# Optimization experiments

Hardware: AMD Instinct MI355X
Metric: run time of the kernel (lower is better)

Reference implementation:

```python
import jax, jax.numpy as jnp
import numpy as np
from jax import lax

N, H, W, C = 4, 64, 64, 256
G, K = 8, 3
Cg = C // G
PAD, STRIDE, DIL = 1, 1, 1
OFFSET_SCALE = 1.0
P = K * K


def setup_inputs() -> dict:
    key = jax.random.key(0)
    ks = jax.random.split(key, 12)
    s = 1.0 / np.sqrt(C)
    return {
        "x": jax.random.normal(ks[0], (N, H, W, C), jnp.float32),
        "in_w": jax.random.normal(ks[1], (C, C), jnp.float32) * s,
        "in_b": jnp.zeros((C,), jnp.float32),
        "out_w": jax.random.normal(ks[2], (C, C), jnp.float32) * s,
        "out_b": jnp.zeros((C,), jnp.float32),
        "off_w": jax.random.normal(ks[3], (C, G * P * 2), jnp.float32) * 0.02,
        "off_b": jax.random.normal(ks[4], (G * P * 2,), jnp.float32) * 0.1,
        "mask_w": jax.random.normal(ks[5], (C, G * P), jnp.float32) * 0.02,
        "mask_b": jnp.zeros((G * P,), jnp.float32),
        "dw_k": jax.random.normal(ks[6], (C, 1, K, K), jnp.float32) * (1.0 / K),
        "bn_g": 1.0 + 0.1 * jax.random.normal(ks[7], (C,), jnp.float32),
        "bn_b": 0.1 * jax.random.normal(ks[8], (C,), jnp.float32),
        "bn_m": 0.1 * jax.random.normal(ks[9], (C,), jnp.float32),
        "bn_v": 1.0 + 0.1 * jax.random.uniform(ks[10], (C,), jnp.float32),
    }


def _bilinear_sample(img, grid):
    # img: [B, Cc, Hi, Wi]; grid: [B, L, P, 2], (x, y) in [-1, 1]
    # grid_sample(mode='bilinear', padding_mode='zeros', align_corners=False)
    B, Cc, Hi, Wi = img.shape
    x = ((grid[..., 0] + 1.0) * Wi - 1.0) * 0.5
    y = ((grid[..., 1] + 1.0) * Hi - 1.0) * 0.5
    x0 = jnp.floor(x)
    y0 = jnp.floor(y)
    fx = x - x0
    fy = y - y0
    x0i = x0.astype(jnp.int32)
    y0i = y0.astype(jnp.int32)
    flat = img.reshape(B, Cc, Hi * Wi)
    gather = jax.vmap(lambda f, i: f[:, i])  # [Cc,HW], [L,P] -> [Cc,L,P]

    def corner(xc, yc, w):
        valid = (xc >= 0) & (xc < Wi) & (yc >= 0) & (yc < Hi)
        idx = jnp.clip(yc, 0, Hi - 1) * Wi + jnp.clip(xc, 0, Wi - 1)
        return gather(flat, idx) * (w * valid)[:, None]

    out = corner(x0i, y0i, (1.0 - fx) * (1.0 - fy))
    out = out + corner(x0i + 1, y0i, fx * (1.0 - fy))
    out = out + corner(x0i, y0i + 1, (1.0 - fx) * fy)
    out = out + corner(x0i + 1, y0i + 1, fx * fy)
    return out  # [B, Cc, L, P]


def reference(x, in_w, in_b, out_w, out_b, off_w, off_b, mask_w, mask_b,
              dw_k, bn_g, bn_b, bn_m, bn_v):
    # input_proj
    xp = x @ in_w + in_b  # [N,H,W,C]

    # depthwise conv (Conv: conv -> BN(inference) -> SiLU) on NCHW
    x1 = jnp.transpose(x, (0, 3, 1, 2))
    x1 = lax.conv_general_dilated(x1, dw_k, (1, 1), [(PAD, PAD), (PAD, PAD)],
                                  feature_group_count=C)
    x1 = (bn_g[:, None, None] * (x1 - bn_m[:, None, None])
          * lax.rsqrt(bn_v + 1e-5)[:, None, None] + bn_b[:, None, None])
    x1 = jax.nn.silu(x1)
    x1 = jnp.transpose(x1, (0, 2, 3, 1))  # NHWC

    offset = x1 @ off_w + off_b  # [N,H,W,G*P*2]
    mask = jax.nn.softmax((x1 @ mask_w + mask_b).reshape(N, H, W, G, P), -1)

    # dcnv3 core: pad input, compute sampling locations, bilinear gather
    Hi, Wi = H + 2 * PAD, W + 2 * PAD
    xpad = jnp.pad(xp, ((0, 0), (PAD, PAD), (PAD, PAD), (0, 0)))

    base = (DIL * (K - 1)) // 2 + 0.5
    ref_y = (base + jnp.arange(H, dtype=jnp.float32) * STRIDE) / Hi
    ref_x = (base + jnp.arange(W, dtype=jnp.float32) * STRIDE) / Wi
    ref = jnp.stack(jnp.meshgrid(ref_x, ref_y, indexing="xy"), -1)  # [H,W,2]

    g1 = jnp.arange(K, dtype=jnp.float32) * DIL - (DIL * (K - 1)) // 2
    gx = jnp.repeat(g1 / Wi, K)  # kx outer (torch meshgrid 'ij' order)
    gy = jnp.tile(g1 / Hi, K)    # ky inner
    grid = jnp.stack([gx, gy], -1)  # [P,2]

    norm = jnp.array([Wi, Hi], jnp.float32)
    loc = (ref[None, :, :, None, None, :]
           + grid[None, None, None, None, :, :] * OFFSET_SCALE
           + offset.reshape(N, H, W, G, P, 2) * (OFFSET_SCALE / norm))
    sgrid = 2.0 * loc - 1.0  # [N,H,W,G,P,2]

    img = xpad.reshape(N, Hi * Wi, G, Cg).transpose(0, 2, 3, 1).reshape(N * G, Cg, Hi, Wi)
    sg = sgrid.reshape(N, H * W, G, P, 2).transpose(0, 2, 1, 3, 4).reshape(N * G, H * W, P, 2)
    samples = _bilinear_sample(img, sg)  # [N*G, Cg, L, P]
    m = mask.reshape(N, H * W, G, P).transpose(0, 2, 1, 3).reshape(N * G, 1, H * W, P)
    out = (samples * m).sum(-1)  # [N*G, Cg, L]
    out = out.reshape(N, C, H * W).transpose(0, 2, 1).reshape(N, H, W, C)
    return out @ out_w + out_b
```

## Files before the change

### kernel.cpp

```cpp
#include <hip/hip_runtime.h>
#include <math.h>

#define NB   4
#define HH   64
#define WW   64
#define CCH  256
#define GG   8
#define CGC  32
#define HI   66
#define NPIX 16384
#define OMWS 256

typedef unsigned short ushort_t;
typedef __attribute__((ext_vector_type(8))) short short8;
typedef __attribute__((ext_vector_type(4))) float floatx4;

__device__ inline ushort_t f2bf(float f) {
    union { float f; unsigned u; } v; v.f = f;
    unsigned r = v.u + 0x7FFF + ((v.u >> 16) & 1);
    return (ushort_t)(r >> 16);
}
__device__ inline float bf2f(ushort_t u) {
    union { unsigned u; float f; } v; v.u = ((unsigned)u) << 16; return v.f;
}

__device__ inline void gload_lds16(const ushort_t* g, ushort_t* l) {
    __builtin_amdgcn_global_load_lds(
        (const __attribute__((address_space(1))) void*)g,
        (__attribute__((address_space(3))) void*)l, 16, 0, 0);
}

template<int MODE>
__device__ __forceinline__
void gemm_body(const ushort_t* __restrict__ A, const ushort_t* __restrict__ Bt,
               const float* __restrict__ bias, void* __restrict__ outv,
               ushort_t* As, ushort_t* Bs, int row0, int col0)
{
    const int tid  = threadIdx.x;
    const int lane = tid & 63, wid = tid >> 6;
    const int q = lane >> 4, r = lane & 15;

    floatx4 acc[2][4] = {};

    auto stage = [&](int buf, int kt) {
        #pragma unroll
        for (int j = 0; j < 4; ++j) {
            int gi = j * 256 + tid;
            int arow = gi >> 3, gk = gi & 7;
            gload_lds16(A + (size_t)(row0 + arow) * 256 + kt * 64 + ((gk ^ (arow & 7)) * 8),
                        &As[buf * 128 * 64 + gi * 8]);
        }
        #pragma unroll
        for (int j = 0; j < 2; ++j) {
            int gi = j * 256 + tid;
            int brow = gi >> 3, gk = gi & 7;
            gload_lds16(Bt + (size_t)(col0 + brow) * 256 + kt * 64 + ((gk ^ (brow & 7)) * 8),
                        &Bs[buf * 64 * 64 + gi * 8]);
        }
    };

    stage(0, 0);
    __syncthreads();
    int cur = 0;
    #pragma unroll 1
    for (int kt = 0; kt < 4; ++kt) {
        if (kt < 3) stage(cur ^ 1, kt + 1);
        #pragma unroll
        for (int kk = 0; kk < 2; ++kk) {
            short8 af[2], bf[4];
            const int gsw = ((kk * 4 + q) ^ (r & 7)) * 8;
            #pragma unroll
            for (int m = 0; m < 2; ++m)
                af[m] = *(const short8*)&As[cur * 128 * 64 + (wid * 32 + m * 16 + r) * 64 + gsw];
            #pragma unroll
            for (int n = 0; n < 4; ++n)
                bf[n] = *(const short8*)&Bs[cur * 64 * 64 + (n * 16 + r) * 64 + gsw];
            #pragma unroll
            for (int m = 0; m < 2; ++m)
                #pragma unroll
                for (int n = 0; n < 4; ++n)
                    acc[m][n] = __builtin_amdgcn_mfma_f32_16x16x32_bf16(
                                    af[m], bf[n], acc[m][n], 0, 0, 0);
        }
        __syncthreads();
        cur ^= 1;
    }

    #pragma unroll
    for (int m = 0; m < 2; ++m) {
        #pragma unroll
        for (int n = 0; n < 4; ++n) {
            #pragma unroll
            for (int j = 0; j < 4; ++j) {
                int row = row0 + wid * 32 + m * 16 + q * 4 + j;
                int col = col0 + n * 16 + r;
                float v = acc[m][n][j] + bias[col];
                if (MODE == 1) {
                    int nn = row >> 12, hh = (row >> 6) & 63, www = row & 63;
                    ((ushort_t*)outv)[(size_t)((nn * HI + hh + 1) * HI + (www + 1)) * CCH + col] = f2bf(v);
                } else if (MODE == 2) {
                    ((ushort_t*)outv)[(size_t)row * 256 + col] = f2bf(v);
                } else {
                    ((float*)outv)[(size_t)row * 256 + col] = v;
                }
            }
        }
    }
}

__device__ __forceinline__ void swz512(int tbid, int& row0, int& col0) {
    int swz = (tbid & 7) * 64 + (tbid >> 3);
    row0 = (swz >> 2) * 128;
    col0 = (swz & 3) * 64;
}

__global__ __launch_bounds__(256)
void gemm_in_off(const ushort_t* __restrict__ xb, const ushort_t* __restrict__ WtIn,
                 const float* __restrict__ in_b, ushort_t* __restrict__ xpadb,
                 const ushort_t* __restrict__ x1b, const ushort_t* __restrict__ W2t,
                 const float* __restrict__ b2, ushort_t* __restrict__ offm)
{
    __shared__ ushort_t As[2 * 128 * 64];
    __shared__ ushort_t Bs[2 * 64 * 64];
    int bid = blockIdx.x;
    int row0, col0;
    if (bid < 512) {
        swz512(bid, row0, col0);
        gemm_body<1>(xb, WtIn, in_b, xpadb, As, Bs, row0, col0);
    } else {
        swz512(bid - 512, row0, col0);
        gemm_body<2>(x1b, W2t, b2, offm, As, Bs, row0, col0);
    }
}

__global__ __launch_bounds__(256)
void gemm_out(const ushort_t* __restrict__ A, const ushort_t* __restrict__ Bt,
              const float* __restrict__ bias, float* __restrict__ out)
{
    __shared__ ushort_t As[2 * 128 * 64];
    __shared__ ushort_t Bs[2 * 64 * 64];
    int row0, col0;
    swz512(blockIdx.x, row0, col0);
    gemm_body<0>(A, Bt, bias, out, As, Bs, row0, col0);
}

__global__ __launch_bounds__(256)
void prep_dw(const float* __restrict__ x,
             const float* __restrict__ in_w, const float* __restrict__ out_w,
             const float* __restrict__ off_w, const float* __restrict__ mask_w,
             const float* __restrict__ off_b, const float* __restrict__ mask_b,
             const float* __restrict__ dw_k, const float* __restrict__ bn_g,
             const float* __restrict__ bn_b, const float* __restrict__ bn_m,
             const float* __restrict__ bn_v,
             ushort_t* __restrict__ xpadb,
             ushort_t* __restrict__ WtIn, ushort_t* __restrict__ WtOut,
             ushort_t* __restrict__ W2t, float* __restrict__ b2,
             ushort_t* __restrict__ x1b, ushort_t* __restrict__ xb)
{
    __shared__ float kT[9][256];
    const int bid = blockIdx.x;
    const int tid = threadIdx.x;

    if (bid < NB * 260) {
        int n = bid / 260, rp = bid % 260;
        int h, w;
        if (rp < 66)       { h = 0;              w = rp; }
        else if (rp < 132) { h = 65;             w = rp - 66; }
        else if (rp < 196) { h = 1 + (rp - 132); w = 0; }
        else               { h = 1 + (rp - 196); w = 65; }
        xpadb[(size_t)((n * HI + h) * HI + w) * CCH + tid] = 0;
        return;
    }
    if (bid < NB * 260 + 256) {
        int n = bid - NB * 260, k = tid;
        WtIn [n * 256 + k] = f2bf(in_w [k * 256 + n]);
        WtOut[n * 256 + k] = f2bf(out_w[k * 256 + n]);
        float w2 = (n < 144) ? off_w[k * 144 + n]
                 : (n < 216) ? mask_w[k * 72 + (n - 144)] : 0.f;
        W2t[n * 256 + k] = f2bf(w2);
        if (k == 0) b2[n] = (n < 144) ? off_b[n] : (n < 216) ? mask_b[n - 144] : 0.f;
        return;
    }

    #pragma unroll
    for (int j = 0; j < 9; ++j) {
        int i = j * 256 + tid;
        kT[i % 9][i / 9] = dw_k[i];
    }
    __syncthreads();

    const int lane = tid & 63, wvid = tid >> 6;
    const int pix = (bid - (NB * 260 + 256)) * 4 + wvid;
    const int n = pix >> 12, hw = pix & 4095, h = hw >> 6, w = hw & 63;
    const int c4 = lane << 2;

    const float4 cv = *reinterpret_cast<const float4*>(x + (size_t)pix * CCH + c4);
    ushort_t xo[4] = { f2bf(cv.x), f2bf(cv.y), f2bf(cv.z), f2bf(cv.w) };
    *reinterpret_cast<ushort4*>(xb + (size_t)pix * CCH + c4) = *reinterpret_cast<ushort4*>(xo);

    const float4 kc = *reinterpret_cast<const float4*>(&kT[4][c4]);
    float ax = cv.x * kc.x, ay = cv.y * kc.y, az = cv.z * kc.z, aw = cv.w * kc.w;

    #pragma unroll
    for (int tap = 0; tap < 9; ++tap) {
        if (tap == 4) continue;
        int hh = h + tap / 3 - 1, ww = w + tap % 3 - 1;
        if ((unsigned)hh < HH && (unsigned)ww < WW) {
            const float4 v = *reinterpret_cast<const float4*>(
                x + (size_t)((n * HH + hh) * WW + ww) * CCH + c4);
            const float4 kk = *reinterpret_cast<const float4*>(&kT[tap][c4]);
            ax += v.x * kk.x; ay += v.y * kk.y; az += v.z * kk.z; aw += v.w * kk.w;
        }
    }
    const float4 g4 = *reinterpret_cast<const float4*>(bn_g + c4);
    const float4 v4 = *reinterpret_cast<const float4*>(bn_v + c4);
    const float4 m4 = *reinterpret_cast<const float4*>(bn_m + c4);
    const float4 bb4 = *reinterpret_cast<const float4*>(bn_b + c4);
    float sx = g4.x * rsqrtf(v4.x + 1e-5f), sy = g4.y * rsqrtf(v4.y + 1e-5f);
    float sz = g4.z * rsqrtf(v4.z + 1e-5f), sw = g4.w * rsqrtf(v4.w + 1e-5f);
    float yx = (ax - m4.x) * sx + bb4.x, yy = (ay - m4.y) * sy + bb4.y;
    float yz = (az - m4.z) * sz + bb4.z, yw = (aw - m4.w) * sw + bb4.w;
    yx = yx / (1.f + __expf(-yx));
    yy = yy / (1.f + __expf(-yy));
    yz = yz / (1.f + __expf(-yz));
    yw = yw / (1.f + __expf(-yw));
    ushort_t o[4] = { f2bf(yx), f2bf(yy), f2bf(yz), f2bf(yw) };
    *reinterpret_cast<ushort4*>(x1b + (size_t)pix * CCH + c4) = *reinterpret_cast<ushort4*>(o);
}

__global__ __launch_bounds__(256)
void dcn_tile(const ushort_t* __restrict__ xpadb, const ushort_t* __restrict__ om,
              ushort_t* __restrict__ coreb)
{
    __shared__ ushort_t win[4 * 256 * 8];
    const int tid = threadIdx.x;
    const int bid = blockIdx.x;
    const int tx = bid & 7, ty = (bid >> 3) & 7, g = (bid >> 6) & 7, n = bid >> 9;
    const int wx0 = tx * 8 - 3, wy0 = ty * 8 - 3;

    {
        const int dy = tid >> 4, dx = tid & 15;
        const int yy = wy0 + dy, xx = wx0 + dx;
        short8 v[4] = {{0,0,0,0,0,0,0,0},{0,0,0,0,0,0,0,0},
                       {0,0,0,0,0,0,0,0},{0,0,0,0,0,0,0,0}};
        if ((unsigned)yy < HI && (unsigned)xx < HI) {
            const ushort_t* src = xpadb + (size_t)((n * HI + yy) * HI + xx) * CCH + g * CGC;
            #pragma unroll
            for (int gr = 0; gr < 4; ++gr)
                v[gr] = *reinterpret_cast<const short8*>(src + gr * 8);
        }
        #pragma unroll
        for (int gr = 0; gr < 4; ++gr)
            *reinterpret_cast<short8*>(&win[(gr * 256 + tid) * 8]) = v[gr];
    }
    __syncthreads();

    const int px = tid >> 2, gr = tid & 3;
    const int h = ty * 8 + (px >> 3), w = tx * 8 + (px & 7);
    const int pix = (n << 12) | (h << 6) | w;
    const ushort_t* __restrict__ omp = om + (size_t)pix * OMWS;

    float lg[9], mx = -1e30f;
    #pragma unroll
    for (int p = 0; p < 9; ++p) { lg[p] = bf2f(omp[144 + g * 9 + p]); mx = fmaxf(mx, lg[p]); }
    float s = 0.f;
    #pragma unroll
    for (int p = 0; p < 9; ++p) { lg[p] = __expf(lg[p] - mx); s += lg[p]; }
    const float inv = 1.f / s;

    float acc[8] = {};
    #pragma unroll
    for (int p = 0; p < 9; ++p) {
        float ox = bf2f(omp[g * 18 + p * 2 + 0]);
        float oy = bf2f(omp[g * 18 + p * 2 + 1]);
        float xi = (float)(w + (p / 3)) + ox;
        float yi = (float)(h + (p % 3)) + oy;
        float x0f = floorf(xi), y0f = floorf(yi);
        int x0 = (int)x0f, y0 = (int)y0f;
        float fx = xi - x0f, fy = yi - y0f;
        float wgt = lg[p] * inv;
        float cw[4] = { (1.f - fx) * (1.f - fy) * wgt, fx * (1.f - fy) * wgt,
                        (1.f - fx) * fy * wgt,         fx * fy * wgt };
        #pragma unroll
        for (int cr = 0; cr < 4; ++cr) {
            int xc = x0 + (cr & 1), yc = y0 + (cr >> 1);
            int sx = xc - wx0, sy = yc - wy0;
            float wc = cw[cr];
            if ((unsigned)sx < 16 && (unsigned)sy < 16) {
                short8 raw = *reinterpret_cast<const short8*>(
                    &win[(gr * 256 + sy * 16 + sx) * 8]);
                #pragma unroll
                for (int j = 0; j < 8; ++j) acc[j] += wc * bf2f((ushort_t)raw[j]);
            } else if ((unsigned)xc < HI && (unsigned)yc < HI) {
                short8 raw = *reinterpret_cast<const short8*>(
                    xpadb + (size_t)((n * HI + yc) * HI + xc) * CCH + g * CGC + gr * 8);
                #pragma unroll
                for (int j = 0; j < 8; ++j) acc[j] += wc * bf2f((ushort_t)raw[j]);
            }
        }
    }
    ushort_t o[8];
    #pragma unroll
    for (int j = 0; j < 8; ++j) o[j] = f2bf(acc[j]);
    *reinterpret_cast<short8*>(coreb + (size_t)pix * CCH + g * CGC + gr * 8) =
        *reinterpret_cast<short8*>(o);
}

extern "C" void kernel_launch(void* const* d_in, const int* in_sizes, int n_in,
                              void* d_out, int out_size, void* d_ws, size_t ws_size,
                              hipStream_t stream) {
    const float* x      = (const float*)d_in[0];
    const float* in_w   = (const float*)d_in[1];
    const float* in_b   = (const float*)d_in[2];
    const float* out_w  = (const float*)d_in[3];
    const float* out_b  = (const float*)d_in[4];
    const float* off_w  = (const float*)d_in[5];
    const float* off_b  = (const float*)d_in[6];
    const float* mask_w = (const float*)d_in[7];
    const float* mask_b = (const float*)d_in[8];
    const float* dw_k   = (const float*)d_in[9];
    const float* bn_g   = (const float*)d_in[10];
    const float* bn_b   = (const float*)d_in[11];
    const float* bn_m   = (const float*)d_in[12];
    const float* bn_v   = (const float*)d_in[13];

    ushort_t* xpadb = (ushort_t*)d_ws;
    ushort_t* xb    = xpadb + 4460544;
    ushort_t* x1b   = xb + 4194304;
    ushort_t* coreb = x1b + 4194304;
    ushort_t* offm  = coreb + 4194304;
    ushort_t* WtIn  = offm + 4194304;
    ushort_t* WtOut = WtIn + 65536;
    ushort_t* W2t   = WtOut + 65536;
    float*    b2    = (float*)(W2t + 65536);

    prep_dw<<<NB * 260 + 256 + NPIX / 4, 256, 0, stream>>>(x,
        in_w, out_w, off_w, mask_w, off_b, mask_b,
        dw_k, bn_g, bn_b, bn_m, bn_v,
        xpadb, WtIn, WtOut, W2t, b2, x1b, xb);

    gemm_in_off<<<1024, 256, 0, stream>>>(xb, WtIn, in_b, xpadb, x1b, W2t, b2, offm);

    dcn_tile<<<NB * GG * 64, 256, 0, stream>>>(xpadb, offm, coreb);

    gemm_out<<<512, 256, 0, stream>>>(coreb, WtOut, out_b, (float*)d_out);
}
```

Before: 58.37 us.

## Fuse offset/mask projection GEMM into deformable sampling kernel

```diff
diff --git a/kernel.cpp b/kernel.cpp
--- a/kernel.cpp
+++ b/kernel.cpp
@@ -9,7 +9,6 @@
 #define CGC  32
 #define HI   66
 #define NPIX 16384
-#define OMWS 256
 
 typedef unsigned short ushort_t;
 typedef __attribute__((ext_vector_type(8))) short short8;
@@ -98,8 +97,6 @@
                 if (MODE == 1) {
                     int nn = row >> 12, hh = (row >> 6) & 63, www = row & 63;
                     ((ushort_t*)outv)[(size_t)((nn * HI + hh + 1) * HI + (www + 1)) * CCH + col] = f2bf(v);
-                } else if (MODE == 2) {
-                    ((ushort_t*)outv)[(size_t)row * 256 + col] = f2bf(v);
                 } else {
                     ((float*)outv)[(size_t)row * 256 + col] = v;
                 }
@@ -115,22 +112,14 @@
 }
 
 __global__ __launch_bounds__(256)
-void gemm_in_off(const ushort_t* __restrict__ xb, const ushort_t* __restrict__ WtIn,
-                 const float* __restrict__ in_b, ushort_t* __restrict__ xpadb,
-                 const ushort_t* __restrict__ x1b, const ushort_t* __restrict__ W2t,
-                 const float* __restrict__ b2, ushort_t* __restrict__ offm)
+void gemm_in(const ushort_t* __restrict__ xb, const ushort_t* __restrict__ WtIn,
+             const float* __restrict__ in_b, ushort_t* __restrict__ xpadb)
 {
     __shared__ ushort_t As[2 * 128 * 64];
     __shared__ ushort_t Bs[2 * 64 * 64];
-    int bid = blockIdx.x;
     int row0, col0;
-    if (bid < 512) {
-        swz512(bid, row0, col0);
-        gemm_body<1>(xb, WtIn, in_b, xpadb, As, Bs, row0, col0);
-    } else {
-        swz512(bid - 512, row0, col0);
-        gemm_body<2>(x1b, W2t, b2, offm, As, Bs, row0, col0);
-    }
+    swz512(blockIdx.x, row0, col0);
+    gemm_body<1>(xb, WtIn, in_b, xpadb, As, Bs, row0, col0);
 }
 
 __global__ __launch_bounds__(256)
@@ -229,14 +218,29 @@
 }
 
 __global__ __launch_bounds__(256)
-void dcn_tile(const ushort_t* __restrict__ xpadb, const ushort_t* __restrict__ om,
+void dcn_tile(const ushort_t* __restrict__ xpadb, const ushort_t* __restrict__ x1b,
+              const ushort_t* __restrict__ W2t, const float* __restrict__ b2,
               ushort_t* __restrict__ coreb)
 {
     __shared__ ushort_t win[4 * 256 * 8];
+    __shared__ ushort_t W2s[32 * 32 * 8];
+    __shared__ float    pL[64 * 33];
+    __shared__ float    b2s[32];
     const int tid = threadIdx.x;
     const int bid = blockIdx.x;
     const int tx = bid & 7, ty = (bid >> 3) & 7, g = (bid >> 6) & 7, n = bid >> 9;
     const int wx0 = tx * 8 - 3, wy0 = ty * 8 - 3;
+
+    #pragma unroll
+    for (int j = 0; j < 4; ++j) {
+        int gi = j * 256 + tid;
+        int row = gi >> 5, pg = gi & 31;
+        int lg = pg ^ (row & 7);
+        int srow = (row < 18) ? g * 18 + row
+                 : (row < 27) ? 144 + g * 9 + (row - 18) : 0;
+        gload_lds16(W2t + (size_t)srow * 256 + lg * 8, W2s + gi * 8);
+    }
+    if (tid < 27) b2s[tid] = b2[tid < 18 ? g * 18 + tid : 144 + g * 9 + (tid - 18)];
 
     {
         const int dy = tid >> 4, dx = tid & 15;
@@ -255,30 +259,64 @@
     }
     __syncthreads();
 
+    {
+        const int lane = tid & 63, wv = tid >> 6;
+        const int q = lane >> 4, r = lane & 15;
+        const int pxl = wv * 16 + r;
+        const int ady = pxl >> 3, adx = pxl & 7;
+        const size_t arow = ((size_t)(n << 12) + (ty * 8 + ady) * 64 + (tx * 8 + adx)) * 256;
+        short8 af[8];
+        #pragma unroll
+        for (int kk = 0; kk < 8; ++kk)
+            af[kk] = *reinterpret_cast<const short8*>(x1b + arow + kk * 32 + q * 8);
+        floatx4 acc[2] = {};
+        #pragma unroll
+        for (int kk = 0; kk < 8; ++kk) {
+            #pragma unroll
+            for (int nt = 0; nt < 2; ++nt) {
+                int row = nt * 16 + r;
+                int pg = (kk * 4 + q) ^ (row & 7);
+                short8 bf = *reinterpret_cast<const short8*>(&W2s[(row * 32 + pg) * 8]);
+                acc[nt] = __builtin_amdgcn_mfma_f32_16x16x32_bf16(af[kk], bf, acc[nt], 0, 0, 0);
+            }
+        }
+        #pragma unroll
+        for (int nt = 0; nt < 2; ++nt) {
+            int nn = nt * 16 + r;
+            float bv = (nn < 27) ? b2s[nn] : 0.f;
+            #pragma unroll
+            for (int j = 0; j < 4; ++j) {
+                int px = wv * 16 + q * 4 + j;
+                pL[px * 33 + nn] = acc[nt][j] + bv;
+            }
+        }
+    }
+    __syncthreads();
+
     const int px = tid >> 2, gr = tid & 3;
     const int h = ty * 8 + (px >> 3), w = tx * 8 + (px & 7);
     const int pix = (n << 12) | (h << 6) | w;
-    const ushort_t* __restrict__ omp = om + (size_t)pix * OMWS;
-
-    float lg[9], mx = -1e30f;
-    #pragma unroll
-    for (int p = 0; p < 9; ++p) { lg[p] = bf2f(omp[144 + g * 9 + p]); mx = fmaxf(mx, lg[p]); }
+    const float* __restrict__ pp = &pL[px * 33];
+
+    float lg9[9], mx = -1e30f;
+    #pragma unroll
+    for (int p = 0; p < 9; ++p) { lg9[p] = pp[18 + p]; mx = fmaxf(mx, lg9[p]); }
     float s = 0.f;
     #pragma unroll
-    for (int p = 0; p < 9; ++p) { lg[p] = __expf(lg[p] - mx); s += lg[p]; }
+    for (int p = 0; p < 9; ++p) { lg9[p] = __expf(lg9[p] - mx); s += lg9[p]; }
     const float inv = 1.f / s;
 
     float acc[8] = {};
     #pragma unroll
     for (int p = 0; p < 9; ++p) {
-        float ox = bf2f(omp[g * 18 + p * 2 + 0]);
-        float oy = bf2f(omp[g * 18 + p * 2 + 1]);
+        float ox = pp[p * 2 + 0];
+        float oy = pp[p * 2 + 1];
         float xi = (float)(w + (p / 3)) + ox;
         float yi = (float)(h + (p % 3)) + oy;
         float x0f = floorf(xi), y0f = floorf(yi);
         int x0 = (int)x0f, y0 = (int)y0f;
         float fx = xi - x0f, fy = yi - y0f;
-        float wgt = lg[p] * inv;
+        float wgt = lg9[p] * inv;
         float cw[4] = { (1.f - fx) * (1.f - fy) * wgt, fx * (1.f - fy) * wgt,
                         (1.f - fx) * fy * wgt,         fx * fy * wgt };
         #pragma unroll
@@ -328,8 +366,7 @@
     ushort_t* xb    = xpadb + 4460544;
     ushort_t* x1b   = xb + 4194304;
     ushort_t* coreb = x1b + 4194304;
-    ushort_t* offm  = coreb + 4194304;
-    ushort_t* WtIn  = offm + 4194304;
+    ushort_t* WtIn  = coreb + 4194304;
     ushort_t* WtOut = WtIn + 65536;
     ushort_t* W2t   = WtOut + 65536;
     float*    b2    = (float*)(W2t + 65536);
@@ -339,9 +376,9 @@
         dw_k, bn_g, bn_b, bn_m, bn_v,
         xpadb, WtIn, WtOut, W2t, b2, x1b, xb);
 
-    gemm_in_off<<<1024, 256, 0, stream>>>(xb, WtIn, in_b, xpadb, x1b, W2t, b2, offm);
-
-    dcn_tile<<<NB * GG * 64, 256, 0, stream>>>(xpadb, offm, coreb);
+    gemm_in<<<512, 256, 0, stream>>>(xb, WtIn, in_b, xpadb);
+
+    dcn_tile<<<NB * GG * 64, 256, 0, stream>>>(xpadb, x1b, W2t, b2, coreb);
 
     gemm_out<<<512, 256, 0, stream>>>(coreb, WtOut, out_b, (float*)d_out);
 }
```

New measurement: 61.53 us. 1.05x slower.

## Enlarge GEMM tiles to 128x128 and regroup offset/mask columns per group

Applied to the files above, without the earlier changes.

```diff
diff --git a/kernel.cpp b/kernel.cpp
--- a/kernel.cpp
+++ b/kernel.cpp
@@ -9,7 +9,6 @@
 #define CGC  32
 #define HI   66
 #define NPIX 16384
-#define OMWS 256
 
 typedef unsigned short ushort_t;
 typedef __attribute__((ext_vector_type(8))) short short8;
@@ -32,15 +31,16 @@
 
 template<int MODE>
 __device__ __forceinline__
-void gemm_body(const ushort_t* __restrict__ A, const ushort_t* __restrict__ Bt,
-               const float* __restrict__ bias, void* __restrict__ outv,
-               ushort_t* As, ushort_t* Bs, int row0, int col0)
+void gemm_body128(const ushort_t* __restrict__ A, const ushort_t* __restrict__ Bt,
+                  const float* __restrict__ bias, void* __restrict__ outv,
+                  ushort_t* As, ushort_t* Bs, int row0, int col0)
 {
     const int tid  = threadIdx.x;
     const int lane = tid & 63, wid = tid >> 6;
+    const int wr = wid >> 1, wc = wid & 1;
     const int q = lane >> 4, r = lane & 15;
 
-    floatx4 acc[2][4] = {};
+    floatx4 acc[4][4] = {};
 
     auto stage = [&](int buf, int kt) {
         #pragma unroll
@@ -51,11 +51,11 @@
                         &As[buf * 128 * 64 + gi * 8]);
         }
         #pragma unroll
-        for (int j = 0; j < 2; ++j) {
+        for (int j = 0; j < 4; ++j) {
             int gi = j * 256 + tid;
             int brow = gi >> 3, gk = gi & 7;
             gload_lds16(Bt + (size_t)(col0 + brow) * 256 + kt * 64 + ((gk ^ (brow & 7)) * 8),
-                        &Bs[buf * 64 * 64 + gi * 8]);
+                        &Bs[buf * 128 * 64 + gi * 8]);
         }
     };
 
@@ -67,16 +67,16 @@
         if (kt < 3) stage(cur ^ 1, kt + 1);
         #pragma unroll
         for (int kk = 0; kk < 2; ++kk) {
-            short8 af[2], bf[4];
+            short8 af[4], bf[4];
             const int gsw = ((kk * 4 + q) ^ (r & 7)) * 8;
             #pragma unroll
-            for (int m = 0; m < 2; ++m)
-                af[m] = *(const short8*)&As[cur * 128 * 64 + (wid * 32 + m * 16 + r) * 64 + gsw];
+            for (int m = 0; m < 4; ++m)
+                af[m] = *(const short8*)&As[cur * 128 * 64 + (wr * 64 + m * 16 + r) * 64 + gsw];
             #pragma unroll
             for (int n = 0; n < 4; ++n)
-                bf[n] = *(const short8*)&Bs[cur * 64 * 64 + (n * 16 + r) * 64 + gsw];
-            #pragma unroll
-            for (int m = 0; m < 2; ++m)
+                bf[n] = *(const short8*)&Bs[cur * 128 * 64 + (wc * 64 + n * 16 + r) * 64 + gsw];
+            #pragma unroll
+            for (int m = 0; m < 4; ++m)
                 #pragma unroll
                 for (int n = 0; n < 4; ++n)
                     acc[m][n] = __builtin_amdgcn_mfma_f32_16x16x32_bf16(
@@ -87,13 +87,13 @@
     }
 
     #pragma unroll
-    for (int m = 0; m < 2; ++m) {
+    for (int m = 0; m < 4; ++m) {
         #pragma unroll
         for (int n = 0; n < 4; ++n) {
             #pragma unroll
             for (int j = 0; j < 4; ++j) {
-                int row = row0 + wid * 32 + m * 16 + q * 4 + j;
-                int col = col0 + n * 16 + r;
+                int row = row0 + wr * 64 + m * 16 + q * 4 + j;
+                int col = col0 + wc * 64 + n * 16 + r;
                 float v = acc[m][n][j] + bias[col];
                 if (MODE == 1) {
                     int nn = row >> 12, hh = (row >> 6) & 63, www = row & 63;
@@ -108,10 +108,10 @@
     }
 }
 
-__device__ __forceinline__ void swz512(int tbid, int& row0, int& col0) {
-    int swz = (tbid & 7) * 64 + (tbid >> 3);
-    row0 = (swz >> 2) * 128;
-    col0 = (swz & 3) * 64;
+__device__ __forceinline__ void swz256(int tbid, int& row0, int& col0) {
+    int swz = (tbid & 7) * 32 + (tbid >> 3);
+    row0 = (swz >> 1) * 128;
+    col0 = (swz & 1) * 128;
 }
 
 __global__ __launch_bounds__(256)
@@ -121,15 +121,15 @@
                  const float* __restrict__ b2, ushort_t* __restrict__ offm)
 {
     __shared__ ushort_t As[2 * 128 * 64];
-    __shared__ ushort_t Bs[2 * 64 * 64];
+    __shared__ ushort_t Bs[2 * 128 * 64];
     int bid = blockIdx.x;
     int row0, col0;
-    if (bid < 512) {
-        swz512(bid, row0, col0);
-        gemm_body<1>(xb, WtIn, in_b, xpadb, As, Bs, row0, col0);
+    if (bid < 256) {
+        swz256(bid, row0, col0);
+        gemm_body128<1>(xb, WtIn, in_b, xpadb, As, Bs, row0, col0);
     } else {
-        swz512(bid - 512, row0, col0);
-        gemm_body<2>(x1b, W2t, b2, offm, As, Bs, row0, col0);
+        swz256(bid - 256, row0, col0);
+        gemm_body128<2>(x1b, W2t, b2, offm, As, Bs, row0, col0);
     }
 }
 
@@ -138,10 +138,10 @@
               const float* __restrict__ bias, float* __restrict__ out)
 {
     __shared__ ushort_t As[2 * 128 * 64];
-    __shared__ ushort_t Bs[2 * 64 * 64];
+    __shared__ ushort_t Bs[2 * 128 * 64];
     int row0, col0;
-    swz512(blockIdx.x, row0, col0);
-    gemm_body<0>(A, Bt, bias, out, As, Bs, row0, col0);
+    swz256(blockIdx.x, row0, col0);
+    gemm_body128<0>(A, Bt, bias, out, As, Bs, row0, col0);
 }
 
 __global__ __launch_bounds__(256)
@@ -175,10 +175,12 @@
         int n = bid - NB * 260, k = tid;
         WtIn [n * 256 + k] = f2bf(in_w [k * 256 + n]);
         WtOut[n * 256 + k] = f2bf(out_w[k * 256 + n]);
-        float w2 = (n < 144) ? off_w[k * 144 + n]
-                 : (n < 216) ? mask_w[k * 72 + (n - 144)] : 0.f;
+        int g = n >> 5, j = n & 31;
+        float w2 = (j < 18) ? off_w[k * 144 + g * 18 + j]
+                 : (j < 27) ? mask_w[k * 72 + g * 9 + (j - 18)] : 0.f;
         W2t[n * 256 + k] = f2bf(w2);
-        if (k == 0) b2[n] = (n < 144) ? off_b[n] : (n < 216) ? mask_b[n - 144] : 0.f;
+        if (k == 0) b2[n] = (j < 18) ? off_b[g * 18 + j]
+                          : (j < 27) ? mask_b[g * 9 + (j - 18)] : 0.f;
         return;
     }
 
@@ -258,27 +260,27 @@
     const int px = tid >> 2, gr = tid & 3;
     const int h = ty * 8 + (px >> 3), w = tx * 8 + (px & 7);
     const int pix = (n << 12) | (h << 6) | w;
-    const ushort_t* __restrict__ omp = om + (size_t)pix * OMWS;
-
-    float lg[9], mx = -1e30f;
-    #pragma unroll
-    for (int p = 0; p < 9; ++p) { lg[p] = bf2f(omp[144 + g * 9 + p]); mx = fmaxf(mx, lg[p]); }
+    const ushort_t* __restrict__ omp = om + (size_t)pix * 256 + g * 32;
+
+    float lg9[9], mx = -1e30f;
+    #pragma unroll
+    for (int p = 0; p < 9; ++p) { lg9[p] = bf2f(omp[18 + p]); mx = fmaxf(mx, lg9[p]); }
     float s = 0.f;
     #pragma unroll
-    for (int p = 0; p < 9; ++p) { lg[p] = __expf(lg[p] - mx); s += lg[p]; }
+    for (int p = 0; p < 9; ++p) { lg9[p] = __expf(lg9[p] - mx); s += lg9[p]; }
     const float inv = 1.f / s;
 
     float acc[8] = {};
     #pragma unroll
     for (int p = 0; p < 9; ++p) {
-        float ox = bf2f(omp[g * 18 + p * 2 + 0]);
-        float oy = bf2f(omp[g * 18 + p * 2 + 1]);
+        float ox = bf2f(omp[p * 2 + 0]);
+        float oy = bf2f(omp[p * 2 + 1]);
         float xi = (float)(w + (p / 3)) + ox;
         float yi = (float)(h + (p % 3)) + oy;
         float x0f = floorf(xi), y0f = floorf(yi);
         int x0 = (int)x0f, y0 = (int)y0f;
         float fx = xi - x0f, fy = yi - y0f;
-        float wgt = lg[p] * inv;
+        float wgt = lg9[p] * inv;
         float cw[4] = { (1.f - fx) * (1.f - fy) * wgt, fx * (1.f - fy) * wgt,
                         (1.f - fx) * fy * wgt,         fx * fy * wgt };
         #pragma unroll
@@ -339,9 +341,9 @@
         dw_k, bn_g, bn_b, bn_m, bn_v,
         xpadb, WtIn, WtOut, W2t, b2, x1b, xb);
 
-    gemm_in_off<<<1024, 256, 0, stream>>>(xb, WtIn, in_b, xpadb, x1b, W2t, b2, offm);
+    gemm_in_off<<<512, 256, 0, stream>>>(xb, WtIn, in_b, xpadb, x1b, W2t, b2, offm);
 
     dcn_tile<<<NB * GG * 64, 256, 0, stream>>>(xpadb, offm, coreb);
 
-    gemm_out<<<512, 256, 0, stream>>>(coreb, WtOut, out_b, (float*)d_out);
-}
+    gemm_out<<<256, 256, 0, stream>>>(coreb, WtOut, out_b, (float*)d_out);
+}
```

Measured after the change: 57.32 us. Within noise of the previous version (-1.8%).
